# Optimization experiments

Hardware: AMD Instinct MI355X
Metric: run time of the kernel (lower is better)

The kernel has to match this reference:

```python
import jax, jax.numpy as jnp
import numpy as np
from jax import lax

N_FEATURES = 160
HIDDEN = 128
NUM_LAYERS = 2
BATCH = 256
SEQ = 512


def _lstm_layer(x, h0, c0, W_ih, W_hh, b_ih, b_hh):
    """Single LSTM layer, batch_first input x: [B, T, D]. Returns hs: [B, T, H].
    PyTorch gate order: i, f, g, o."""
    b = b_ih + b_hh  # [4H]

    def step(carry, xt):
        h, c = carry
        gates = xt @ W_ih.T + h @ W_hh.T + b  # [B, 4H]
        i, f, g, o = jnp.split(gates, 4, axis=-1)
        i = jax.nn.sigmoid(i)
        f = jax.nn.sigmoid(f)
        g = jnp.tanh(g)
        o = jax.nn.sigmoid(o)
        c = f * c + i * g
        h = o * jnp.tanh(c)
        return (h, c), h

    xs = jnp.swapaxes(x, 0, 1)  # [T, B, D]
    (_, _), hs = lax.scan(step, (h0, c0), xs)
    return jnp.swapaxes(hs, 0, 1)  # [B, T, H]


def setup_inputs() -> dict:
    key = jax.random.key(0)
    ks = jax.random.split(key, 9)
    s = 1.0 / np.sqrt(HIDDEN)  # PyTorch LSTM init scale
    x = jax.random.normal(ks[0], (BATCH, SEQ, N_FEATURES), dtype=jnp.float32)
    h0 = jnp.zeros((NUM_LAYERS, BATCH, HIDDEN), dtype=jnp.float32)
    c0 = jnp.zeros((NUM_LAYERS, BATCH, HIDDEN), dtype=jnp.float32)
    return {
        "x": x,
        "h0": h0,
        "c0": c0,
        "W_ih0": jax.random.uniform(ks[1], (4 * HIDDEN, N_FEATURES), jnp.float32, -s, s),
        "W_hh0": jax.random.uniform(ks[2], (4 * HIDDEN, HIDDEN), jnp.float32, -s, s),
        "b_ih0": jax.random.uniform(ks[3], (4 * HIDDEN,), jnp.float32, -s, s),
        "b_hh0": jax.random.uniform(ks[4], (4 * HIDDEN,), jnp.float32, -s, s),
        "W_ih1": jax.random.uniform(ks[5], (4 * HIDDEN, HIDDEN), jnp.float32, -s, s),
        "W_hh1": jax.random.uniform(ks[6], (4 * HIDDEN, HIDDEN), jnp.float32, -s, s),
        "b_ih1": jax.random.uniform(ks[7], (4 * HIDDEN,), jnp.float32, -s, s),
        "b_hh1": jax.random.uniform(ks[8], (4 * HIDDEN,), jnp.float32, -s, s),
    }


def reference(x, h0, c0, W_ih0, W_hh0, b_ih0, b_hh0, W_ih1, W_hh1, b_ih1, b_hh1):
    h1 = _lstm_layer(x, h0[0], c0[0], W_ih0, W_hh0, b_ih0, b_hh0)   # [B, T, H]
    h2 = _lstm_layer(h1, h0[1], c0[1], W_ih1, W_hh1, b_ih1, b_hh1)  # [B, T, H]
    return h2[:, -1:, :]  # [B, 1, H]
```

## Files before the change

kernel.cpp:

```cpp
#include <hip/hip_runtime.h>


typedef _Float16 f16;
typedef _Float16 f16x8 __attribute__((ext_vector_type(8)));
typedef float f32x4 __attribute__((ext_vector_type(4)));

#define B_  256
#define T_  512
#define HID 128
#define NG  512
#define KX0 160
#define NC  4
#define TC  128

static __device__ __forceinline__ unsigned pack2(float a, float b) {
  union { f16 h[2]; unsigned u; } v;
  v.h[0] = (f16)a; v.h[1] = (f16)b;
  return v.u;
}

static __device__ __forceinline__ float dot2f(unsigned a, unsigned b, float c) {
  float d;
  asm("v_dot2_f32_f16 %0, %1, %2, %3" : "=v"(d) : "v"(a), "v"(b), "v"(c));
  return d;
}

static __device__ __forceinline__ float fast_rcp(float x) {
#if __has_builtin(__builtin_amdgcn_rcpf)
  return __builtin_amdgcn_rcpf(x);
#else
  return 1.0f / x;
#endif
}
static __device__ __forceinline__ float fast_exp2(float x) {
#if __has_builtin(__builtin_amdgcn_exp2f)
  return __builtin_amdgcn_exp2f(x);
#else
  return exp2f(x);
#endif
}
static __device__ __forceinline__ float sigm(float x) {
  return fast_rcp(1.0f + fast_exp2(x * -1.44269504f));
}
static __device__ __forceinline__ float tanh_f(float x) {
  float e = fast_exp2(x * 2.885390082f);
  return 1.0f - 2.0f * fast_rcp(e + 1.0f);
}

static __device__ __forceinline__ float qp_add1(float v) {
  int iv = __builtin_bit_cast(int, v);
  int t = __builtin_amdgcn_update_dpp(iv, iv, 0xB1, 0xF, 0xF, true);
  return v + __builtin_bit_cast(float, t);
}

static __device__ __forceinline__ float gxval(const uint4& g, int j) {
  unsigned w = (j >> 1) == 0 ? g.x : (j >> 1) == 1 ? g.y : (j >> 1) == 2 ? g.z : g.w;
  unsigned hs = (j & 1) ? (w >> 16) : (w & 0xffffu);
  f16 v = __builtin_bit_cast(f16, (unsigned short)hs);
  return (float)v;
}

template <int K, bool AF16>
__global__ __launch_bounds__(256) void gemm_xw(
    const void* __restrict__ Aptr, size_t bStride,
    const float* __restrict__ W,
    const float* __restrict__ bihp, const float* __restrict__ bhhp,
    f16* __restrict__ D) {
  constexpr int KP = K + 8;
  __shared__ f16 As[128][KP];
  __shared__ f16 Bs[64][KP];
  const int tid = threadIdx.x;
  const int mtile = blockIdx.x, ntile = blockIdx.y;

  if (AF16) {
    const f16* A = (const f16*)Aptr;
    for (int i = tid; i < 128 * (K / 8); i += 256) {
      int r = i / (K / 8), kk = (i % (K / 8)) * 8;
      size_t grow = (size_t)mtile * 128 + r;
      uint4 v = *(const uint4*)(A + grow * K + kk);
      *(uint4*)&As[r][kk] = v;
    }
  } else {
    const float* A = (const float*)Aptr;
    for (int i = tid; i < 128 * (K / 4); i += 256) {
      int r = i / (K / 4), kk = (i % (K / 4)) * 4;
      int grow = mtile * 128 + r;
      int bb = grow >> 7, tt = grow & (TC - 1);
      const float* p = A + (size_t)bb * bStride + (size_t)tt * K + kk;
      float4 v = *(const float4*)p;
      uint2 u;
      u.x = pack2(v.x, v.y);
      u.y = pack2(v.z, v.w);
      *(uint2*)&As[r][kk] = u;
    }
  }
  for (int i = tid; i < 64 * (K / 4); i += 256) {
    int r = i / (K / 4), kk = (i % (K / 4)) * 4;
    const float* p = W + (size_t)(ntile * 64 + r) * K + kk;
    float4 v = *(const float4*)p;
    uint2 u;
    u.x = pack2(v.x, v.y);
    u.y = pack2(v.z, v.w);
    *(uint2*)&Bs[r][kk] = u;
  }
  __syncthreads();

  const int w = tid >> 6, l = tid & 63;
  const int lr = l & 15, lg = l >> 4;
  f32x4 acc[2][4] = {};
#pragma unroll
  for (int ks = 0; ks < K / 32; ++ks) {
    f16x8 a0 = *(const f16x8*)&As[w * 32 + lr][ks * 32 + lg * 8];
    f16x8 a1 = *(const f16x8*)&As[w * 32 + 16 + lr][ks * 32 + lg * 8];
    f16x8 bf[4];
#pragma unroll
    for (int nj = 0; nj < 4; ++nj)
      bf[nj] = *(const f16x8*)&Bs[nj * 16 + lr][ks * 32 + lg * 8];
#pragma unroll
    for (int nj = 0; nj < 4; ++nj) {
      acc[0][nj] = __builtin_amdgcn_mfma_f32_16x16x32_f16(a0, bf[nj], acc[0][nj], 0, 0, 0);
      acc[1][nj] = __builtin_amdgcn_mfma_f32_16x16x32_f16(a1, bf[nj], acc[1][nj], 0, 0, 0);
    }
  }
#pragma unroll
  for (int mi = 0; mi < 2; ++mi) {
#pragma unroll
    for (int nj = 0; nj < 4; ++nj) {
      int col = ntile * 64 + nj * 16 + lr;
      float bsum = bihp[col] + bhhp[col];
      int cell = col & 127, gate = col >> 7;
      int rowbase = mtile * 128 + w * 32 + mi * 16 + lg * 4;
      int bb = rowbase >> 7, tt = rowbase & (TC - 1);
      unsigned lo = pack2(acc[mi][nj][0] + bsum, acc[mi][nj][1] + bsum);
      unsigned hi = pack2(acc[mi][nj][2] + bsum, acc[mi][nj][3] + bsum);
      size_t idx = (((size_t)bb * HID + cell) * 4 + gate) * TC + tt;
      uint2 u; u.x = lo; u.y = hi;
      *(uint2*)(D + idx) = u;
    }
  }
}

struct RecArgs {
  const f16* Gx;
  const float* Whh;
  const float* hin; const float* cin;
  float* hst; float* cst;
  f16* h1out;
  float* fin;
};

__global__ __launch_bounds__(256) void lstm_rec2(RecArgs A, RecArgs B, int nA) {
  const RecArgs& P = ((int)blockIdx.x < nA) ? A : B;
  const int b = ((int)blockIdx.x < nA) ? blockIdx.x : blockIdx.x - nA;
  const int tid = threadIdx.x;
  const int c = tid >> 1, s = tid & 1;
  __shared__ unsigned hbuf[2][64];

  unsigned wh[4][32];
#pragma unroll
  for (int g = 0; g < 4; ++g) {
    const int r = g * HID + c;
#pragma unroll
    for (int j = 0; j < 32; ++j) {
      int p = 32 * s + j;
      wh[g][j] = pack2(P.Whh[(size_t)r * HID + 2 * p], P.Whh[(size_t)r * HID + 2 * p + 1]);
    }
  }
  float cstate = P.cin[b * HID + c];
  if (tid < 64)
    hbuf[0][tid] = pack2(P.hin[b * HID + 2 * tid], P.hin[b * HID + 2 * tid + 1]);

  const f16* gxb = P.Gx + ((size_t)b * HID + c) * 4 * TC;
  f16* h1x = P.h1out ? P.h1out + (size_t)b * TC * HID + c : (f16*)nullptr;
  __syncthreads();

  float hprev = 0.f;

#pragma unroll 1
  for (int t0 = 0; t0 < TC; t0 += 8) {
    uint4 g4[4];
#pragma unroll
    for (int g = 0; g < 4; ++g) g4[g] = *(const uint4*)(gxb + (size_t)g * TC + t0);

#pragma unroll
    for (int j = 0; j < 8; ++j) {
      const int t = t0 + j;
      if (h1x && s == 0 && (j > 0 || t0 > 0)) h1x[(size_t)(t - 1) * HID] = (f16)hprev;
      const uint4* hs4 = (const uint4*)&hbuf[t & 1][32 * s];
      float ai = 0.f, af = 0.f, ag = 0.f, ao = 0.f;
#pragma unroll
      for (int k = 0; k < 8; ++k) {
        uint4 v = hs4[k];
        ai = dot2f(v.x, wh[0][4 * k + 0], ai); ai = dot2f(v.y, wh[0][4 * k + 1], ai);
        ai = dot2f(v.z, wh[0][4 * k + 2], ai); ai = dot2f(v.w, wh[0][4 * k + 3], ai);
        af = dot2f(v.x, wh[1][4 * k + 0], af); af = dot2f(v.y, wh[1][4 * k + 1], af);
        af = dot2f(v.z, wh[1][4 * k + 2], af); af = dot2f(v.w, wh[1][4 * k + 3], af);
        ag = dot2f(v.x, wh[2][4 * k + 0], ag); ag = dot2f(v.y, wh[2][4 * k + 1], ag);
        ag = dot2f(v.z, wh[2][4 * k + 2], ag); ag = dot2f(v.w, wh[2][4 * k + 3], ag);
        ao = dot2f(v.x, wh[3][4 * k + 0], ao); ao = dot2f(v.y, wh[3][4 * k + 1], ao);
        ao = dot2f(v.z, wh[3][4 * k + 2], ao); ao = dot2f(v.w, wh[3][4 * k + 3], ao);
      }
      ai = qp_add1(ai); af = qp_add1(af); ag = qp_add1(ag); ao = qp_add1(ao);

      float iv = sigm(ai + gxval(g4[0], j));
      float fv = sigm(af + gxval(g4[1], j));
      float gv = tanh_f(ag + gxval(g4[2], j));
      float ov = sigm(ao + gxval(g4[3], j));
      cstate = fv * cstate + iv * gv;
      float h = ov * tanh_f(cstate);
      if (s == 0) ((f16*)&hbuf[(t + 1) & 1][0])[c] = (f16)h;
      hprev = h;
      __syncthreads();
    }
  }

  if (h1x && s == 0) h1x[(size_t)(TC - 1) * HID] = (f16)hprev;
  if (s == 0) {
    P.hst[b * HID + c] = (float)(f16)hprev;
    P.cst[b * HID + c] = cstate;
    if (P.fin) P.fin[b * HID + c] = hprev;
  }
}

extern "C" void kernel_launch(void* const* d_in, const int* in_sizes, int n_in,
                              void* d_out, int out_size, void* d_ws,
                              size_t ws_size, hipStream_t stream) {
  const float* x    = (const float*)d_in[0];
  const float* h0   = (const float*)d_in[1];
  const float* c0   = (const float*)d_in[2];
  const float* Wih0 = (const float*)d_in[3];
  const float* Whh0 = (const float*)d_in[4];
  const float* bih0 = (const float*)d_in[5];
  const float* bhh0 = (const float*)d_in[6];
  const float* Wih1 = (const float*)d_in[7];
  const float* Whh1 = (const float*)d_in[8];
  const float* bih1 = (const float*)d_in[9];
  const float* bhh1 = (const float*)d_in[10];

  char* w = (char*)d_ws;
  f16* Gx0 = (f16*)w;      w += (size_t)B_ * TC * NG * 2;
  f16* Gx1 = (f16*)w;      w += (size_t)B_ * TC * NG * 2;
  f16* h1  = (f16*)w;      w += (size_t)B_ * TC * HID * 2;
  float* sH0 = (float*)w;  w += (size_t)B_ * HID * 4;
  float* sC0 = (float*)w;  w += (size_t)B_ * HID * 4;
  float* sH1 = (float*)w;  w += (size_t)B_ * HID * 4;
  float* sC1 = (float*)w;

  const dim3 ggrid(B_ * TC / 128, 8);

  auto l0args = [&](int cc) {
    RecArgs a;
    a.Gx = Gx0; a.Whh = Whh0;
    a.hin = cc == 0 ? h0 : sH0; a.cin = cc == 0 ? c0 : sC0;
    a.hst = sH0; a.cst = sC0; a.h1out = h1; a.fin = nullptr;
    return a;
  };
  auto l1args = [&](int cc) {
    RecArgs a;
    a.Gx = Gx1; a.Whh = Whh1;
    a.hin = cc == 0 ? h0 + B_ * HID : sH1; a.cin = cc == 0 ? c0 + B_ * HID : sC1;
    a.hst = sH1; a.cst = sC1; a.h1out = nullptr;
    a.fin = cc == NC - 1 ? (float*)d_out : nullptr;
    return a;
  };

  RecArgs dummy = {};

  gemm_xw<KX0, false><<<ggrid, 256, 0, stream>>>(
      x + (size_t)0 * TC * KX0, (size_t)T_ * KX0, Wih0, bih0, bhh0, Gx0);
  lstm_rec2<<<B_, 256, 0, stream>>>(l0args(0), dummy, B_);

  for (int cc = 1; cc < NC; ++cc) {
    gemm_xw<HID, true><<<ggrid, 256, 0, stream>>>(h1, 0, Wih1, bih1, bhh1, Gx1);
    gemm_xw<KX0, false><<<ggrid, 256, 0, stream>>>(
        x + (size_t)cc * TC * KX0, (size_t)T_ * KX0, Wih0, bih0, bhh0, Gx0);
    lstm_rec2<<<2 * B_, 256, 0, stream>>>(l0args(cc), l1args(cc - 1), B_);
  }

  gemm_xw<HID, true><<<ggrid, 256, 0, stream>>>(h1, 0, Wih1, bih1, bhh1, Gx1);
  lstm_rec2<<<B_, 256, 0, stream>>>(l1args(NC - 1), dummy, B_);
}
```

Before: 886.1 us.

## Double-buffer gate prefetch, split dot-product chains, lighten per-step barrier in LSTM recurrence

```diff
diff --git a/kernel.cpp b/kernel.cpp
--- a/kernel.cpp
+++ b/kernel.cpp
@@ -12,6 +12,8 @@
 #define KX0 160
 #define NC  4
 #define TC  128
+
+#define STEP_BARRIER() asm volatile("s_waitcnt lgkmcnt(0)\n\ts_barrier" ::: "memory")
 
 static __device__ __forceinline__ unsigned pack2(float a, float b) {
   union { f16 h[2]; unsigned u; } v;
@@ -149,7 +151,8 @@
   float* fin;
 };
 
-__global__ __launch_bounds__(256) void lstm_rec2(RecArgs A, RecArgs B, int nA) {
+__global__ __launch_bounds__(256) __attribute__((amdgpu_waves_per_eu(1, 1)))
+void lstm_rec2(RecArgs A, RecArgs B, int nA) {
   const RecArgs& P = ((int)blockIdx.x < nA) ? A : B;
   const int b = ((int)blockIdx.x < nA) ? blockIdx.x : blockIdx.x - nA;
   const int tid = threadIdx.x;
@@ -172,46 +175,63 @@
 
   const f16* gxb = P.Gx + ((size_t)b * HID + c) * 4 * TC;
   f16* h1x = P.h1out ? P.h1out + (size_t)b * TC * HID + c : (f16*)nullptr;
+
+  uint4 gA[4], gB[4];
+#pragma unroll
+  for (int g = 0; g < 4; ++g) gA[g] = *(const uint4*)(gxb + (size_t)g * TC + 0);
   __syncthreads();
 
   float hprev = 0.f;
 
+  auto STEP = [&](const uint4 (&gx)[4], int t, int j) {
+    if (h1x && s == 0 && t > 0) h1x[(size_t)(t - 1) * HID] = (f16)hprev;
+    const uint4* hs4 = (const uint4*)&hbuf[t & 1][32 * s];
+    float acc[4][4] = {{0.f, 0.f, 0.f, 0.f}, {0.f, 0.f, 0.f, 0.f},
+                       {0.f, 0.f, 0.f, 0.f}, {0.f, 0.f, 0.f, 0.f}};
+#pragma unroll
+    for (int k = 0; k < 8; ++k) {
+      uint4 v = hs4[k];
+#pragma unroll
+      for (int g = 0; g < 4; ++g) {
+        acc[g][0] = dot2f(v.x, wh[g][4 * k + 0], acc[g][0]);
+        acc[g][1] = dot2f(v.y, wh[g][4 * k + 1], acc[g][1]);
+        acc[g][2] = dot2f(v.z, wh[g][4 * k + 2], acc[g][2]);
+        acc[g][3] = dot2f(v.w, wh[g][4 * k + 3], acc[g][3]);
+      }
+    }
+    float ai = (acc[0][0] + acc[0][1]) + (acc[0][2] + acc[0][3]);
+    float af = (acc[1][0] + acc[1][1]) + (acc[1][2] + acc[1][3]);
+    float ag = (acc[2][0] + acc[2][1]) + (acc[2][2] + acc[2][3]);
+    float ao = (acc[3][0] + acc[3][1]) + (acc[3][2] + acc[3][3]);
+    ai = qp_add1(ai); af = qp_add1(af); ag = qp_add1(ag); ao = qp_add1(ao);
+
+    float iv = sigm(ai + gxval(gx[0], j));
+    float fv = sigm(af + gxval(gx[1], j));
+    float gv = tanh_f(ag + gxval(gx[2], j));
+    float ov = sigm(ao + gxval(gx[3], j));
+    cstate = fv * cstate + iv * gv;
+    float h = ov * tanh_f(cstate);
+    if (s == 0) ((f16*)&hbuf[(t + 1) & 1][0])[c] = (f16)h;
+    hprev = h;
+    STEP_BARRIER();
+  };
+
 #pragma unroll 1
-  for (int t0 = 0; t0 < TC; t0 += 8) {
-    uint4 g4[4];
-#pragma unroll
-    for (int g = 0; g < 4; ++g) g4[g] = *(const uint4*)(gxb + (size_t)g * TC + t0);
-
-#pragma unroll
-    for (int j = 0; j < 8; ++j) {
-      const int t = t0 + j;
-      if (h1x && s == 0 && (j > 0 || t0 > 0)) h1x[(size_t)(t - 1) * HID] = (f16)hprev;
-      const uint4* hs4 = (const uint4*)&hbuf[t & 1][32 * s];
-      float ai = 0.f, af = 0.f, ag = 0.f, ao = 0.f;
-#pragma unroll
-      for (int k = 0; k < 8; ++k) {
-        uint4 v = hs4[k];
-        ai = dot2f(v.x, wh[0][4 * k + 0], ai); ai = dot2f(v.y, wh[0][4 * k + 1], ai);
-        ai = dot2f(v.z, wh[0][4 * k + 2], ai); ai = dot2f(v.w, wh[0][4 * k + 3], ai);
-        af = dot2f(v.x, wh[1][4 * k + 0], af); af = dot2f(v.y, wh[1][4 * k + 1], af);
-        af = dot2f(v.z, wh[1][4 * k + 2], af); af = dot2f(v.w, wh[1][4 * k + 3], af);
-        ag = dot2f(v.x, wh[2][4 * k + 0], ag); ag = dot2f(v.y, wh[2][4 * k + 1], ag);
-        ag = dot2f(v.z, wh[2][4 * k + 2], ag); ag = dot2f(v.w, wh[2][4 * k + 3], ag);
-        ao = dot2f(v.x, wh[3][4 * k + 0], ao); ao = dot2f(v.y, wh[3][4 * k + 1], ao);
-        ao = dot2f(v.z, wh[3][4 * k + 2], ao); ao = dot2f(v.w, wh[3][4 * k + 3], ao);
-      }
-      ai = qp_add1(ai); af = qp_add1(af); ag = qp_add1(ag); ao = qp_add1(ao);
-
-      float iv = sigm(ai + gxval(g4[0], j));
-      float fv = sigm(af + gxval(g4[1], j));
-      float gv = tanh_f(ag + gxval(g4[2], j));
-      float ov = sigm(ao + gxval(g4[3], j));
-      cstate = fv * cstate + iv * gv;
-      float h = ov * tanh_f(cstate);
-      if (s == 0) ((f16*)&hbuf[(t + 1) & 1][0])[c] = (f16)h;
-      hprev = h;
-      __syncthreads();
-    }
+  for (int t0 = 0; t0 < TC; t0 += 16) {
+    {
+      int tn = t0 + 8;
+#pragma unroll
+      for (int g = 0; g < 4; ++g) gB[g] = *(const uint4*)(gxb + (size_t)g * TC + tn);
+    }
+#pragma unroll
+    for (int j = 0; j < 8; ++j) STEP(gA, t0 + j, j);
+    {
+      int tm = t0 + 16; if (tm > TC - 8) tm = TC - 8;
+#pragma unroll
+      for (int g = 0; g < 4; ++g) gA[g] = *(const uint4*)(gxb + (size_t)g * TC + tm);
+    }
+#pragma unroll
+    for (int j = 0; j < 8; ++j) STEP(gB, t0 + 8 + j, j);
   }
 
   if (h1x && s == 0) h1x[(size_t)(TC - 1) * HID] = (f16)hprev;
```

Measured after the change: 904.7 us. 2.1% more time.
